# Optimization experiments

Measured on AMD Instinct MI355X. Metric: run time of the kernel, lower is better.

Reference implementation:

```python
import jax, jax.numpy as jnp
import numpy as np

MINI_BLOCK = 4

def setup_inputs() -> dict:
    key = jax.random.key(0)
    k1, k2 = jax.random.split(key)
    B, IN, OUT = 4096, 4096, 4096
    gy, gx = OUT // MINI_BLOCK, IN // MINI_BLOCK
    x = jax.random.normal(k1, (B, IN), dtype=jnp.float32)
    eigens = jax.random.normal(k2, (gy, gx, MINI_BLOCK), dtype=jnp.float32)
    return {"x": x, "eigens": eigens}

def reference(x, eigens):
    # Block-circulant linear: out[b, y, :] = sum_x circconv(eigens[y, x], x_blk[b, x])
    # computed in the frequency domain. Original code used two-sided rfft +
    # complex_mult + irfft per (b, y, x) block and summed over x; since the FFT
    # and complex product are linear, we contract over x in frequency space
    # with an einsum instead of materializing the (B, gy, gx, block) tensor.
    gy, gx, blk = eigens.shape
    xb = x.reshape(-1, gx, blk)                      # (B, gx, blk)
    f_eig = jnp.fft.rfft(eigens, axis=-1)            # (gy, gx, blk//2+1) complex
    f_x = jnp.fft.rfft(xb, axis=-1)                  # (B, gx, blk//2+1)
    f_out = jnp.einsum('yxk,bxk->byk', f_eig, f_x)   # contract over gx
    out = jnp.fft.irfft(f_out, n=blk, axis=-1)       # (B, gy, blk)
    return out.reshape(-1, gy * blk)
```

## Files before the change

### kernel.cpp

```cpp
#include <hip/hip_runtime.h>


typedef __attribute__((ext_vector_type(8))) short bf16x8_t;
typedef __attribute__((ext_vector_type(4))) float f32x4_t;

#define NDIM 4096
#define TILE 128
#define BK 32

__device__ __forceinline__ unsigned short f2bf(float f) {
    unsigned int u = __builtin_bit_cast(unsigned int, f);
    u += 0x7fffu + ((u >> 16) & 1u);
    return (unsigned short)(u >> 16);
}

__device__ __forceinline__ void async_copy16(const void* g, void* l) {
    __builtin_amdgcn_global_load_lds(
        (const __attribute__((address_space(1))) void*)g,
        (__attribute__((address_space(3))) void*)l,
        16, 0, 0);
}


__global__ __launch_bounds__(256) void pre_k(const float* __restrict__ x,
                                             const float* __restrict__ eig,
                                             unsigned short* __restrict__ xp,
                                             unsigned short* __restrict__ B) {
    const int t = threadIdx.x;
    if (blockIdx.x < 4096) {
        int gid = blockIdx.x * 256 + t;
        int b = gid >> 8, j0 = (gid & 255) << 2;
        const float4* src = (const float4*)x + ((size_t)b << 10) + j0;
        unsigned short S[4], R[4], Mi[4], Z[4], T[4];
#pragma unroll
        for (int q = 0; q < 4; ++q) {
            float4 v = src[q];
            float r = v.x - v.z, m = v.w - v.y;
            S[q]  = f2bf(r + m);
            R[q]  = f2bf(r);
            Mi[q] = f2bf(m);
            Z[q]  = f2bf(v.x + v.y + v.z + v.w);
            T[q]  = f2bf(v.x - v.y + v.z - v.w);
        }
        unsigned short* dst = xp + (size_t)b * 5120 + j0;
        *(ushort4*)(dst)        = *(const ushort4*)S;
        *(ushort4*)(dst + 1024) = *(const ushort4*)R;
        *(ushort4*)(dst + 2048) = *(const ushort4*)Mi;
        *(ushort4*)(dst + 3072) = *(const ushort4*)Z;
        *(ushort4*)(dst + 4096) = *(const ushort4*)T;
    } else {
        int gid = (blockIdx.x - 4096) * 256 + t;
        int y = gid >> 8, c0 = (gid & 255) << 2;
        const float4* src = (const float4*)eig + ((size_t)y << 10) + c0;
        unsigned short P0[4], P1[4], P2[4], P3[4], P4[4];
#pragma unroll
        for (int q = 0; q < 4; ++q) {
            float4 v = src[q];
            float r = v.x - v.z, m = v.w - v.y;
            P0[q] = f2bf(r);
            P1[q] = f2bf(m - r);
            P2[q] = f2bf(-(m + r));
            P3[q] = f2bf(v.x + v.y + v.z + v.w);
            P4[q] = f2bf(v.x - v.y + v.z - v.w);
        }
        unsigned short* dst = B + (size_t)y * 5120 + c0;
        *(ushort4*)(dst)        = *(const ushort4*)P0;
        *(ushort4*)(dst + 1024) = *(const ushort4*)P1;
        *(ushort4*)(dst + 2048) = *(const ushort4*)P2;
        *(ushort4*)(dst + 3072) = *(const ushort4*)P3;
        *(ushort4*)(dst + 4096) = *(const ushort4*)P4;
    }
}

__global__ __launch_bounds__(512, 2) void gemm_f(
        const unsigned short* __restrict__ A,
        const unsigned short* __restrict__ B,
        float* __restrict__ C) {
    __shared__ unsigned short sm[3][16384];

    const int raw    = blockIdx.x;
    const int xcd    = raw & 7;
    const int idx    = raw >> 3;
    const int rowBlk = xcd * 4 + (idx >> 3);
    const int colBlk = idx & 7;

    const int t    = threadIdx.x;
    const int lane = t & 63;
    const int w    = t >> 6;
    const int wm   = (w >> 2) * 64;
    const int wn   = (w & 3) * 32;
    const int lr   = lane & 15;
    const int quad = lane >> 4;
    const int xr   = lr & 7;

    const int srow = t >> 3;
    const int scol = ((t & 7) ^ ((t >> 3) & 7)) << 3;
    const unsigned short* pa0 = A + (size_t)(rowBlk * 128 + srow) * 5120 + scol;
    const unsigned short* pa1 = pa0 + (size_t)64 * 5120;
    const unsigned short* pb0 = B + (size_t)(colBlk * 128 + srow) * 5120 + scol;
    const unsigned short* pb1 = pb0 + (size_t)64 * 5120;

    char* smb  = (char*)&sm[0][0];
    char* dstT = smb + (size_t)t * 16;

    int koff = 0;

    f32x4_t aK1[4][2] = {};
    f32x4_t aOi[4][2];
    f32x4_t aO0[4][2] = {};
    f32x4_t aO2[4][2] = {};

#define STAGE_F(BOFF)                                          \
    {                                                          \
        char* d = dstT + (BOFF);                               \
        async_copy16(pa0 + koff, d);                           \
        async_copy16(pa1 + koff, d + 8192);                    \
        async_copy16(pb0 + koff, d + 16384);                   \
        async_copy16(pb1 + koff, d + 24576);                   \
        koff += 64;                                            \
    }

#define COMPUTE_F(BOFF, ACC)                                                  \
    {                                                                         \
        const char* ab = smb + (BOFF) + (wm + lr) * 128;                      \
        const char* bb = smb + (BOFF) + 16384 + (wn + lr) * 128;              \
        _Pragma("unroll")                                                     \
        for (int kk = 0; kk < 2; ++kk) {                                      \
            const int sw = ((((kk << 2) | quad)) ^ xr) << 4;                  \
            bf16x8_t af[4], bfv[2];                                           \
            _Pragma("unroll")                                                 \
            for (int i = 0; i < 4; ++i)                                       \
                af[i] = *(const bf16x8_t*)(ab + i * 2048 + sw);               \
            _Pragma("unroll")                                                 \
            for (int j = 0; j < 2; ++j)                                       \
                bfv[j] = *(const bf16x8_t*)(bb + j * 2048 + sw);              \
            __builtin_amdgcn_s_setprio(1);                                    \
            _Pragma("unroll")                                                 \
            for (int mt = 0; mt < 4; ++mt)                                    \
                _Pragma("unroll")                                             \
                for (int nt = 0; nt < 2; ++nt)                                \
                    ACC[mt][nt] = __builtin_amdgcn_mfma_f32_16x16x32_bf16(    \
                        af[mt], bfv[nt], ACC[mt][nt], 0, 0, 0);               \
            __builtin_amdgcn_s_setprio(0);                                    \
        }                                                                     \
    }

#define STEP_F(ACC)                                            \
    {                                                          \
        asm volatile("s_waitcnt vmcnt(4)" ::: "memory");       \
        __builtin_amdgcn_s_barrier();                          \
        __builtin_amdgcn_sched_barrier(0);                     \
        int sb_ = cb + 65536;                                  \
        if (sb_ >= 98304) sb_ -= 98304;                        \
        if (koff < 5120) STAGE_F(sb_);                         \
        COMPUTE_F(cb, ACC);                                    \
        cb += 32768;                                           \
        if (cb >= 98304) cb = 0;                               \
    }

#define PHASE_F(ACC, NSTEP)                                    \
    _Pragma("unroll 1")                                        \
    for (int s2 = 0; s2 < (NSTEP); ++s2) STEP_F(ACC)

    STAGE_F(0);
    STAGE_F(32768);
    int cb = 0;

    PHASE_F(aK1, 16)
#pragma unroll
    for (int mt = 0; mt < 4; ++mt)
#pragma unroll
        for (int nt = 0; nt < 2; ++nt) aOi[mt][nt] = aK1[mt][nt];
    PHASE_F(aOi, 16)
    PHASE_F(aK1, 16)
    PHASE_F(aO0, 16)
    PHASE_F(aO2, 15)

    asm volatile("s_waitcnt vmcnt(0)" ::: "memory");
    __builtin_amdgcn_s_barrier();
    __builtin_amdgcn_sched_barrier(0);
    COMPUTE_F(cb, aO2);

#undef PHASE_F
#undef STEP_F
#undef COMPUTE_F
#undef STAGE_F

    const int orow0 = rowBlk * 128 + wm + quad * 4;
    const int yc0   = colBlk * 128 + wn + lr;
#pragma unroll
    for (int mt = 0; mt < 4; ++mt) {
#pragma unroll
        for (int r = 0; r < 4; ++r) {
            float* dst = C + (size_t)(orow0 + mt * 16 + r) * NDIM;
#pragma unroll
            for (int nt = 0; nt < 2; ++nt) {
                int yc = yc0 + nt * 16;
                float O0 = aO0[mt][nt][r], Or = aK1[mt][nt][r];
                float Oi = aOi[mt][nt][r], O2 = aO2[mt][nt][r];
                float4 o;
                o.x = 0.25f * (O0 + 2.0f * Or + O2);
                o.y = 0.25f * (O0 - 2.0f * Oi - O2);
                o.z = 0.25f * (O0 - 2.0f * Or + O2);
                o.w = 0.25f * (O0 + 2.0f * Oi - O2);
                *(float4*)(dst + 4 * yc) = o;
            }
        }
    }
}


__global__ __launch_bounds__(256) void fwd_x_fb(const float* __restrict__ x,
                                                unsigned short* __restrict__ xp) {
    int gid = blockIdx.x * 256 + threadIdx.x;
    int b = gid >> 10, j = gid & 1023;
    float4 v = ((const float4*)x)[(size_t)b * 1024 + j];
    unsigned short* dst = xp + (size_t)b * NDIM + j;
    dst[0]    = f2bf(v.x + v.y + v.z + v.w);
    dst[1024] = f2bf(v.x - v.z);
    dst[2048] = f2bf(v.w - v.y);
    dst[3072] = f2bf(v.x - v.y + v.z - v.w);
}

__global__ __launch_bounds__(256) void build_b_fb(const float* __restrict__ eig,
                                                  unsigned short* __restrict__ B) {
    int gid = blockIdx.x * 256 + threadIdx.x;
    int y = gid >> 10, c = gid & 1023;
    float4 v = ((const float4*)eig)[(size_t)y * 1024 + c];
    float r = v.x - v.z, s = v.w - v.y;
    B[(size_t)y * 1024 + c] = f2bf(v.x + v.y + v.z + v.w);
    unsigned short* b1r = B + 1048576 + (size_t)y * 2048;
    b1r[c]        = f2bf(r);
    b1r[1024 + c] = f2bf(-s);
    unsigned short* b1i = B + 3145728 + (size_t)y * 2048;
    b1i[c]        = f2bf(s);
    b1i[1024 + c] = f2bf(r);
    B[5242880 + (size_t)y * 1024 + c] = f2bf(v.x - v.y + v.z - v.w);
}

__global__ __launch_bounds__(256, 2) void gemm_fb(
        const unsigned short* __restrict__ A,
        const unsigned short* __restrict__ B,
        float* __restrict__ C) {
    __shared__ unsigned short lA[TILE * BK];
    __shared__ unsigned short lB[TILE * BK];

    const int Ks[4]   = {1024, 2048, 2048, 1024};
    const int Aoff[4] = {0, 1024, 1024, 3072};
    const size_t Boff[4] = {0u, 1048576u, 3145728u, 5242880u};

    int lin = blockIdx.x;
    int seg, nseg, blkM;
    if (lin < 512) { seg = 1 + ((lin >> 3) & 1); nseg = lin & 7; blkM = lin >> 4; }
    else { int i = lin - 512; seg = ((i >> 3) & 1) * 3; nseg = i & 7; blkM = i >> 4; }

    const int K    = Ks[seg];
    const int aoff = Aoff[seg];
    const unsigned short* Bs = B + Boff[seg];

    const int t    = threadIdx.x;
    const int lane = t & 63;
    const int w    = t >> 6;
    const int wm   = (w >> 1) * 64;
    const int wn   = (w & 1) * 64;
    const int lr   = lane & 15;
    const int quad = lane >> 4;

    const int e0 = t * 8;
    const int r0 = e0 >> 5;
    const int c0 = e0 & 31;

    const unsigned short* pa0 = A + (size_t)(blkM * TILE + r0) * NDIM + aoff + c0;
    const unsigned short* pa1 = pa0 + (size_t)64 * NDIM;
    const unsigned short* pb0 = Bs + (size_t)(nseg * TILE + r0) * K + c0;
    const unsigned short* pb1 = pb0 + (size_t)64 * K;

    unsigned short* dA0 = &lA[e0];
    unsigned short* dA1 = &lA[2048 + e0];
    unsigned short* dB0 = &lB[e0];
    unsigned short* dB1 = &lB[2048 + e0];

    const unsigned short* la0 = &lA[(wm + lr) * BK + quad * 8];
    const unsigned short* lb0 = &lB[(wn + lr) * BK + quad * 8];

    f32x4_t acc[4][4] = {};

    for (int k0 = 0; k0 < K; k0 += BK) {
        async_copy16(pa0 + k0, dA0);
        async_copy16(pa1 + k0, dA1);
        async_copy16(pb0 + k0, dB0);
        async_copy16(pb1 + k0, dB1);
        asm volatile("s_waitcnt vmcnt(0)" ::: "memory");
        __syncthreads();

        bf16x8_t af[4], bfr[4];
#pragma unroll
        for (int i = 0; i < 4; ++i)
            af[i] = *(const bf16x8_t*)(la0 + i * 16 * BK);
#pragma unroll
        for (int i = 0; i < 4; ++i)
            bfr[i] = *(const bf16x8_t*)(lb0 + i * 16 * BK);

#pragma unroll
        for (int mt = 0; mt < 4; ++mt)
#pragma unroll
            for (int nt = 0; nt < 4; ++nt)
                acc[mt][nt] = __builtin_amdgcn_mfma_f32_16x16x32_bf16(
                    af[mt], bfr[nt], acc[mt][nt], 0, 0, 0);

        __syncthreads();
    }

    const int orow0 = blkM * TILE + wm + quad * 4;
    const int ocol0 = seg * 1024 + nseg * TILE + wn + lr;
#pragma unroll
    for (int mt = 0; mt < 4; ++mt) {
#pragma unroll
        for (int r = 0; r < 4; ++r) {
            float* dst = C + (size_t)(orow0 + mt * 16 + r) * NDIM + ocol0;
#pragma unroll
            for (int nt = 0; nt < 4; ++nt)
                dst[nt * 16] = acc[mt][nt][r];
        }
    }
}

__global__ __launch_bounds__(256) void post_fb(float* __restrict__ O) {
    float* row = O + (size_t)blockIdx.x * NDIM;
    const int t = threadIdx.x;
    float4 v0 = *(const float4*)(row + 4 * t);
    float4 vr = *(const float4*)(row + 1024 + 4 * t);
    float4 vi = *(const float4*)(row + 2048 + 4 * t);
    float4 v2 = *(const float4*)(row + 3072 + 4 * t);
    __syncthreads();
    const float* a0 = (const float*)&v0;
    const float* ar = (const float*)&vr;
    const float* ai = (const float*)&vi;
    const float* a2 = (const float*)&v2;
#pragma unroll
    for (int i = 0; i < 4; ++i) {
        float4 o;
        o.x = 0.25f * (a0[i] + 2.0f * ar[i] + a2[i]);
        o.y = 0.25f * (a0[i] - 2.0f * ai[i] - a2[i]);
        o.z = 0.25f * (a0[i] - 2.0f * ar[i] + a2[i]);
        o.w = 0.25f * (a0[i] + 2.0f * ai[i] - a2[i]);
        *(float4*)(row + 16 * t + 4 * i) = o;
    }
}


extern "C" void kernel_launch(void* const* d_in, const int* in_sizes, int n_in,
                              void* d_out, int out_size, void* d_ws, size_t ws_size,
                              hipStream_t stream) {
    const float* x   = (const float*)d_in[0];
    const float* eig = (const float*)d_in[1];
    float* out = (float*)d_out;

    const size_t NEED = (size_t)50 * 1024 * 1024;

    if (ws_size >= NEED) {
        unsigned short* Xp = (unsigned short*)d_ws;
        unsigned short* Bp = (unsigned short*)((char*)d_ws + 41943040u);

        pre_k<<<5120, 256, 0, stream>>>(x, eig, Xp, Bp);
        gemm_f<<<256, 512, 0, stream>>>(Xp, Bp, out);
    } else {
        unsigned short* Xp = (unsigned short*)d_ws;
        unsigned short* Bp = Xp + (size_t)NDIM * NDIM;

        fwd_x_fb<<<(NDIM * 1024) / 256, 256, 0, stream>>>(x, Xp);
        build_b_fb<<<(1024 * 1024) / 256, 256, 0, stream>>>(eig, Bp);
        gemm_fb<<<dim3(1024, 1), 256, 0, stream>>>(Xp, Bp, out);
        post_fb<<<NDIM, 256, 0, stream>>>(out);
    }
}
```

Measured before the change: 184.0 us.

## Halve gemm workgroup to 4 waves with 64x64 warp tiles, spill partials to output

The main GEMM now runs 256 threads per block instead of 512, so each wave computes a 64x64 tile instead of 64x32. Each thread issues eight async loads per stage instead of four, and the vmcnt wait rises to match. Holding four accumulator sets would need too many registers, so only two are kept. The first two finished frequency components are written to the output buffer as scratch and read back before the final combine. This trades fewer waves and fewer LDS fragment reloads per MFMA for less latency hiding and extra global write and read traffic. The scratch write relies on the same rows and columns of C being written and read by the same block.

Measured after the change: 190.6 us. 3.6% more time.

```diff
diff --git a/kernel.cpp b/kernel.cpp
--- a/kernel.cpp
+++ b/kernel.cpp
@@ -72,7 +72,7 @@
     }
 }
 
-__global__ __launch_bounds__(512, 2) void gemm_f(
+__global__ __launch_bounds__(256, 1) void gemm_f(
         const unsigned short* __restrict__ A,
         const unsigned short* __restrict__ B,
         float* __restrict__ C) {
@@ -87,117 +87,163 @@
     const int t    = threadIdx.x;
     const int lane = t & 63;
     const int w    = t >> 6;
-    const int wm   = (w >> 2) * 64;
-    const int wn   = (w & 3) * 32;
+    const int wm   = (w >> 1) * 64;
+    const int wn   = (w & 1) * 64;
     const int lr   = lane & 15;
     const int quad = lane >> 4;
     const int xr   = lr & 7;
 
     const int srow = t >> 3;
-    const int scol = ((t & 7) ^ ((t >> 3) & 7)) << 3;
-    const unsigned short* pa0 = A + (size_t)(rowBlk * 128 + srow) * 5120 + scol;
-    const unsigned short* pa1 = pa0 + (size_t)64 * 5120;
-    const unsigned short* pb0 = B + (size_t)(colBlk * 128 + srow) * 5120 + scol;
-    const unsigned short* pb1 = pb0 + (size_t)64 * 5120;
+    const int scol = ((t & 7) ^ (srow & 7)) << 3;
+    const unsigned short* paw = A + (size_t)(rowBlk * 128 + srow) * 5120 + scol;
+    const unsigned short* pbw = B + (size_t)(colBlk * 128 + srow) * 5120 + scol;
+    const unsigned short* pa0 = paw;
+    const unsigned short* pa1 = paw + (size_t)32 * 5120;
+    const unsigned short* pa2 = paw + (size_t)64 * 5120;
+    const unsigned short* pa3 = paw + (size_t)96 * 5120;
+    const unsigned short* pb0 = pbw;
+    const unsigned short* pb1 = pbw + (size_t)32 * 5120;
+    const unsigned short* pb2 = pbw + (size_t)64 * 5120;
+    const unsigned short* pb3 = pbw + (size_t)96 * 5120;
 
     char* smb  = (char*)&sm[0][0];
-    char* dstT = smb + (size_t)t * 16;
+    char* dstT = smb + srow * 128 + (t & 7) * 16;
 
     int koff = 0;
 
-    f32x4_t aK1[4][2] = {};
-    f32x4_t aOi[4][2];
-    f32x4_t aO0[4][2] = {};
-    f32x4_t aO2[4][2] = {};
-
-#define STAGE_F(BOFF)                                          \
+    f32x4_t accA[4][4] = {};
+    f32x4_t accB[4][4] = {};
+
+#define STAGE4(BOFF)                                           \
     {                                                          \
         char* d = dstT + (BOFF);                               \
         async_copy16(pa0 + koff, d);                           \
-        async_copy16(pa1 + koff, d + 8192);                    \
+        async_copy16(pa1 + koff, d + 4096);                    \
+        async_copy16(pa2 + koff, d + 8192);                    \
+        async_copy16(pa3 + koff, d + 12288);                   \
         async_copy16(pb0 + koff, d + 16384);                   \
-        async_copy16(pb1 + koff, d + 24576);                   \
+        async_copy16(pb1 + koff, d + 20480);                   \
+        async_copy16(pb2 + koff, d + 24576);                   \
+        async_copy16(pb3 + koff, d + 28672);                   \
         koff += 64;                                            \
     }
 
-#define COMPUTE_F(BOFF, ACC)                                                  \
+#define COMPUTE4(BOFF, ACC)                                                   \
     {                                                                         \
         const char* ab = smb + (BOFF) + (wm + lr) * 128;                      \
         const char* bb = smb + (BOFF) + 16384 + (wn + lr) * 128;              \
         _Pragma("unroll")                                                     \
         for (int kk = 0; kk < 2; ++kk) {                                      \
             const int sw = ((((kk << 2) | quad)) ^ xr) << 4;                  \
-            bf16x8_t af[4], bfv[2];                                           \
+            bf16x8_t af[4], bfv[4];                                           \
             _Pragma("unroll")                                                 \
             for (int i = 0; i < 4; ++i)                                       \
                 af[i] = *(const bf16x8_t*)(ab + i * 2048 + sw);               \
             _Pragma("unroll")                                                 \
-            for (int j = 0; j < 2; ++j)                                       \
+            for (int j = 0; j < 4; ++j)                                       \
                 bfv[j] = *(const bf16x8_t*)(bb + j * 2048 + sw);              \
             __builtin_amdgcn_s_setprio(1);                                    \
             _Pragma("unroll")                                                 \
             for (int mt = 0; mt < 4; ++mt)                                    \
                 _Pragma("unroll")                                             \
-                for (int nt = 0; nt < 2; ++nt)                                \
+                for (int nt = 0; nt < 4; ++nt)                                \
                     ACC[mt][nt] = __builtin_amdgcn_mfma_f32_16x16x32_bf16(    \
                         af[mt], bfv[nt], ACC[mt][nt], 0, 0, 0);               \
             __builtin_amdgcn_s_setprio(0);                                    \
         }                                                                     \
     }
 
-#define STEP_F(ACC)                                            \
+#define STEP4(ACC)                                             \
     {                                                          \
-        asm volatile("s_waitcnt vmcnt(4)" ::: "memory");       \
+        asm volatile("s_waitcnt vmcnt(8)" ::: "memory");       \
         __builtin_amdgcn_s_barrier();                          \
         __builtin_amdgcn_sched_barrier(0);                     \
         int sb_ = cb + 65536;                                  \
         if (sb_ >= 98304) sb_ -= 98304;                        \
-        if (koff < 5120) STAGE_F(sb_);                         \
-        COMPUTE_F(cb, ACC);                                    \
+        if (koff < 5120) STAGE4(sb_);                          \
+        COMPUTE4(cb, ACC);                                     \
         cb += 32768;                                           \
         if (cb >= 98304) cb = 0;                               \
     }
 
-#define PHASE_F(ACC, NSTEP)                                    \
+#define PHASE4(ACC, NSTEP)                                     \
     _Pragma("unroll 1")                                        \
-    for (int s2 = 0; s2 < (NSTEP); ++s2) STEP_F(ACC)
-
-    STAGE_F(0);
-    STAGE_F(32768);
+    for (int s2 = 0; s2 < (NSTEP); ++s2) STEP4(ACC)
+
+    STAGE4(0);
+    STAGE4(32768);
     int cb = 0;
 
-    PHASE_F(aK1, 16)
+    PHASE4(accA, 16)
 #pragma unroll
     for (int mt = 0; mt < 4; ++mt)
 #pragma unroll
-        for (int nt = 0; nt < 2; ++nt) aOi[mt][nt] = aK1[mt][nt];
-    PHASE_F(aOi, 16)
-    PHASE_F(aK1, 16)
-    PHASE_F(aO0, 16)
-    PHASE_F(aO2, 15)
+        for (int nt = 0; nt < 4; ++nt) accB[mt][nt] = accA[mt][nt];
+    PHASE4(accB, 16)
+    PHASE4(accA, 16)
+
+    const int prow0   = rowBlk * 128 + wm + quad * 4;
+    const int colBase = colBlk * 512;
+    const int lc      = wn + lr;
+#pragma unroll
+    for (int mt = 0; mt < 4; ++mt) {
+#pragma unroll
+        for (int r = 0; r < 4; ++r) {
+            float* pr = C + (size_t)(prow0 + mt * 16 + r) * NDIM + colBase;
+#pragma unroll
+            for (int nt = 0; nt < 4; ++nt) {
+                pr[lc + nt * 16]       = accA[mt][nt][r];
+                pr[128 + lc + nt * 16] = accB[mt][nt][r];
+            }
+        }
+    }
+    {
+        f32x4_t z = {0.f, 0.f, 0.f, 0.f};
+#pragma unroll
+        for (int mt = 0; mt < 4; ++mt)
+#pragma unroll
+            for (int nt = 0; nt < 4; ++nt) { accA[mt][nt] = z; accB[mt][nt] = z; }
+    }
+
+    PHASE4(accA, 16)
+    PHASE4(accB, 15)
 
     asm volatile("s_waitcnt vmcnt(0)" ::: "memory");
     __builtin_amdgcn_s_barrier();
     __builtin_amdgcn_sched_barrier(0);
-    COMPUTE_F(cb, aO2);
-
-#undef PHASE_F
-#undef STEP_F
-#undef COMPUTE_F
-#undef STAGE_F
-
-    const int orow0 = rowBlk * 128 + wm + quad * 4;
-    const int yc0   = colBlk * 128 + wn + lr;
+    COMPUTE4(cb, accB);
+
+#undef PHASE4
+#undef STEP4
+#undef COMPUTE4
+#undef STAGE4
+
+    float por[4][4][4], poi[4][4][4];
 #pragma unroll
     for (int mt = 0; mt < 4; ++mt) {
 #pragma unroll
         for (int r = 0; r < 4; ++r) {
-            float* dst = C + (size_t)(orow0 + mt * 16 + r) * NDIM;
-#pragma unroll
-            for (int nt = 0; nt < 2; ++nt) {
-                int yc = yc0 + nt * 16;
-                float O0 = aO0[mt][nt][r], Or = aK1[mt][nt][r];
-                float Oi = aOi[mt][nt][r], O2 = aO2[mt][nt][r];
+            const float* pr = C + (size_t)(prow0 + mt * 16 + r) * NDIM + colBase;
+#pragma unroll
+            for (int nt = 0; nt < 4; ++nt) {
+                por[mt][nt][r] = pr[lc + nt * 16];
+                poi[mt][nt][r] = pr[128 + lc + nt * 16];
+            }
+        }
+    }
+    asm volatile("s_waitcnt vmcnt(0)" ::: "memory");
+    __builtin_amdgcn_s_barrier();
+
+#pragma unroll
+    for (int mt = 0; mt < 4; ++mt) {
+#pragma unroll
+        for (int r = 0; r < 4; ++r) {
+            float* dst = C + (size_t)(prow0 + mt * 16 + r) * NDIM;
+#pragma unroll
+            for (int nt = 0; nt < 4; ++nt) {
+                int yc = colBlk * 128 + wn + nt * 16 + lr;
+                float O0 = accA[mt][nt][r], O2 = accB[mt][nt][r];
+                float Or = por[mt][nt][r], Oi = poi[mt][nt][r];
                 float4 o;
                 o.x = 0.25f * (O0 + 2.0f * Or + O2);
                 o.y = 0.25f * (O0 - 2.0f * Oi - O2);
@@ -363,7 +409,7 @@
         unsigned short* Bp = (unsigned short*)((char*)d_ws + 41943040u);
 
         pre_k<<<5120, 256, 0, stream>>>(x, eig, Xp, Bp);
-        gemm_f<<<256, 512, 0, stream>>>(Xp, Bp, out);
+        gemm_f<<<256, 256, 0, stream>>>(Xp, Bp, out);
     } else {
         unsigned short* Xp = (unsigned short*)d_ws;
         unsigned short* Bp = Xp + (size_t)NDIM * NDIM;
```
